# Kernel tuning notes

Measured on AMD Instinct MI355X. Metric: run time of the kernel, lower is better.

The kernel has to match this reference:

```python
import math
import jax, jax.numpy as jnp
import numpy as np

B, T, D, H = 4, 2048, 1024, 16
HD = D // H


def setup_inputs() -> dict:
    key = jax.random.key(0)
    ks = jax.random.split(key, 5)
    s = 1.0 / math.sqrt(D)  # linear-layer-ish init scale
    x = jax.random.normal(ks[0], (B, T, D), dtype=jnp.float32)
    wq = jax.random.normal(ks[1], (D, D), dtype=jnp.float32) * s
    wk = jax.random.normal(ks[2], (D, D), dtype=jnp.float32) * s
    wv = jax.random.normal(ks[3], (D, D), dtype=jnp.float32) * s
    wo = jax.random.normal(ks[4], (D, D), dtype=jnp.float32) * s
    bq = jnp.zeros((D,), jnp.float32)
    bk = jnp.zeros((D,), jnp.float32)
    bv = jnp.zeros((D,), jnp.float32)
    bo = jnp.zeros((D,), jnp.float32)
    # causal 0/1 mask, broadcast over batch and heads: [1, 1, T, T]
    mask = jnp.tril(jnp.ones((T, T), jnp.int32))[None, None]
    return {"x": x, "wq": wq, "bq": bq, "wk": wk, "bk": bk,
            "wv": wv, "bv": bv, "wo": wo, "bo": bo, "mask": mask}


def reference(x, wq, bq, wk, bk, wv, bv, wo, bo, mask):
    b, t, d = x.shape
    # separate QKV linears (x_cond defaults to x -> self-attention)
    q = x @ wq.T + bq
    k = x @ wk.T + bk
    v = x @ wv.T + bv
    # [b, t, h, hd] -> [b, h, t, hd]
    q = q.reshape(b, t, H, HD).transpose(0, 2, 1, 3)
    k = k.reshape(b, t, H, HD).transpose(0, 2, 1, 3)
    v = v.reshape(b, t, H, HD).transpose(0, 2, 1, 3)
    scale = 1.0 / math.sqrt(HD)
    attn = jnp.einsum('bhtd,bhsd->bhts', q, k) * scale  # [b, h, t, t]
    attn = jnp.where(mask[:, :, :t, :t] == 0, jnp.float32(-jnp.inf), attn)
    attn = jax.nn.softmax(attn, axis=-1)
    # dropout is identity in eval mode
    out = jnp.einsum('bhts,bhsd->bhtd', attn, v)  # [b, h, t, hd]
    out = out.transpose(0, 2, 1, 3).reshape(b, t, d)
    return out @ wo.T + bo
```

## Files before the change

kernel.cpp:

```cpp
#include <hip/hip_runtime.h>
#include <cstdint>

typedef __bf16 bf16x8 __attribute__((ext_vector_type(8)));
typedef float f32x4 __attribute__((ext_vector_type(4)));
typedef uint32_t u32x4 __attribute__((ext_vector_type(4)));
typedef unsigned short u16;

#define B_ 4
#define T_ 2048
#define D_ 1024
#define H_ 16
#define HD_ 64
#define M_ (B_*T_)
#define QSCALE 0.1803368801111204f

__device__ __forceinline__ u16 f2bf(float f) {
  union { float f; uint32_t u; } x; x.f = f;
  uint32_t u = x.u;
  uint32_t r = (u + 0x7FFFu + ((u >> 16) & 1u)) >> 16;
  return (u16)r;
}

__device__ __forceinline__ uint32_t pkbf(float a, float b) {
  union { float f; uint32_t u; } x, y; x.f = a; y.f = b;
  uint32_t t0 = x.u + 0x8000u, t1 = y.u + 0x8000u;
  return __builtin_amdgcn_perm(t1, t0, 0x07060302u);
}

__device__ __forceinline__ bf16x8 ld8(const u16* p) {
  return *(const bf16x8*)p;
}

__device__ __forceinline__ void gl_lds16(const u16* g, u16* l) {
  __builtin_amdgcn_global_load_lds(
      (__attribute__((address_space(1))) void*)(g),
      (__attribute__((address_space(3))) void*)(l), 16, 0, 0);
}

__global__ void cvt_all(const float* __restrict__ x, const float* __restrict__ wq,
                        const float* __restrict__ wk, const float* __restrict__ wv,
                        const float* __restrict__ wo,
                        u16* __restrict__ xb, u16* __restrict__ wqb, u16* __restrict__ wkb,
                        u16* __restrict__ wvb, u16* __restrict__ wob) {
  const long NX = (long)M_ * D_;
  long i = ((long)blockIdx.x * 256 + threadIdx.x) * 4;
  const float* s; u16* d; long j;
  if (i < NX) { s = x; d = xb; j = i; }
  else {
    long r = i - NX; int seg = (int)(r >> 20); j = r & ((1 << 20) - 1);
    s = seg == 0 ? wq : seg == 1 ? wk : seg == 2 ? wv : wo;
    d = seg == 0 ? wqb : seg == 1 ? wkb : seg == 2 ? wvb : wob;
  }
  float4 v = *(const float4*)(s + j);
  ushort4 o;
  o.x = f2bf(v.x); o.y = f2bf(v.y); o.z = f2bf(v.z); o.w = f2bf(v.w);
  *(ushort4*)(d + j) = o;
}


__device__ __forceinline__ void ldA_all(bf16x8 (&af)[4][2], const u16* buf,
                                        int wr, int lanem, int quad) {
#pragma unroll
  for (int mi = 0; mi < 4; ++mi)
#pragma unroll
    for (int ks = 0; ks < 2; ++ks) {
      int row = wr * 64 + mi * 16 + lanem;
      int off = row * 64 + ((ks * 32 + quad * 8) ^ ((lanem & 7) << 3));
      af[mi][ks] = ld8(buf + off);
    }
}

__device__ __forceinline__ void ldB_all(bf16x8 (&bfr)[4][2], const u16* buf,
                                        int wc, int lanem, int quad) {
#pragma unroll
  for (int nj = 0; nj < 4; ++nj)
#pragma unroll
    for (int ks = 0; ks < 2; ++ks) {
      int row = 256 + wc * 64 + nj * 16 + lanem;
      int off = row * 64 + ((ks * 32 + quad * 8) ^ ((lanem & 7) << 3));
      bfr[nj][ks] = ld8(buf + off);
    }
}

__device__ __forceinline__ void mfmaAll(f32x4 (&acc)[4][4], const bf16x8 (&af)[4][2],
                                        const bf16x8 (&bfr)[4][2]) {
#pragma unroll
  for (int mi = 0; mi < 4; ++mi)
#pragma unroll
    for (int nj = 0; nj < 4; ++nj)
#pragma unroll
      for (int ks = 0; ks < 2; ++ks)
        acc[mi][nj] = __builtin_amdgcn_mfma_f32_16x16x32_bf16(
            af[mi][ks], bfr[nj][ks], acc[mi][nj], 0, 0, 0);
}

#define GEMM_V5_KLOOP(Asrc, Bsrc)                                              \
  u16* p0 = &sm.S[0][0][0];                                                    \
  u16* p1 = &sm.S[1][0][0];                                                    \
  u16* p2 = &sm.S[2][0][0];                                                    \
  auto stage = [&](u16* bufbase, int u, int k0) {                              \
    const u16* src = (u < 4)                                                   \
        ? Asrc + (size_t)(m0 + u * 64 + wv * 8 + grow) * D_ + k0 + gcol        \
        : Bsrc + (size_t)(n0 + (u - 4) * 64 + wv * 8 + grow) * D_ + k0 + gcol; \
    gl_lds16(src, bufbase + (u * 64 + wv * 8) * 64);                           \
  };                                                                           \
  _Pragma("unroll")                                                            \
  for (int u = 0; u < 6; ++u) stage(p0, u, 0);                                 \
  _Pragma("unroll")                                                            \
  for (int u = 0; u < 6; ++u) stage(p1, u, 64);                                \
  asm volatile("s_waitcnt vmcnt(6)" ::: "memory");                             \
  __builtin_amdgcn_s_barrier();                                                \
  for (int kt = 0; kt < 16; ++kt) {                                            \
    const int k2 = (kt + 2) << 6;                                              \
    ldA_all(af, p0, wr, lanem, quad);                                          \
    ldB_all(bfr, p0, wc, lanem, quad);                                         \
    if (kt < 14) {                                                             \
      stage(p2, 0, k2); stage(p2, 1, k2); stage(p2, 2, k2);                    \
      stage(p2, 3, k2); stage(p2, 4, k2); stage(p2, 5, k2);                    \
    }                                                                          \
    asm volatile("s_waitcnt lgkmcnt(0)" ::: "memory");                         \
    __builtin_amdgcn_sched_barrier(0);                                         \
    __builtin_amdgcn_s_setprio(1);                                             \
    mfmaAll(acc, af, bfr);                                                     \
    __builtin_amdgcn_s_setprio(0);                                             \
    __builtin_amdgcn_sched_barrier(0);                                         \
    if (kt < 14)       asm volatile("s_waitcnt vmcnt(6)" ::: "memory");        \
    else if (kt == 14) asm volatile("s_waitcnt vmcnt(0)" ::: "memory");        \
    __builtin_amdgcn_s_barrier();                                              \
    u16* t = p0; p0 = p1; p1 = p2; p2 = t;                                     \
  }

__global__ __launch_bounds__(512, 2)
void gemm_qkv(const u16* __restrict__ A, const u16* __restrict__ Bw,
              const float* __restrict__ bq, const float* __restrict__ bk,
              const float* __restrict__ bv,
              u16* __restrict__ qb, u16* __restrict__ kb, u16* __restrict__ vtb) {
  __shared__ union {
    u16 S[3][384][64];
    u16 C[256 * 136];
  } sm;

  const int tid = threadIdx.x;
  const int wv = tid >> 6, lane = tid & 63;
  const int lanem = lane & 15, quad = lane >> 4;
  const int wr = wv >> 1, wc = wv & 1;

  const int l = ((int)blockIdx.x & 7) * 96 + ((int)blockIdx.x >> 3);
  const int n0 = (l % 24) * 128, m0 = (l / 24) * 256;

  const int grow = lane >> 3;
  const int gcol = (((lane & 7) ^ grow) * 8);

  f32x4 acc[4][4];
#pragma unroll
  for (int a = 0; a < 4; ++a)
#pragma unroll
    for (int b = 0; b < 4; ++b) acc[a][b] = (f32x4){0.f, 0.f, 0.f, 0.f};

  bf16x8 af[4][2];
  bf16x8 bfr[4][2];

  GEMM_V5_KLOOP(A, Bw);

  const int seg = n0 >> 10, n0l = n0 & 1023;
  const int bb = m0 >> 11, tl0 = m0 & (T_ - 1);

  if (seg == 2) {
    __syncthreads();
#pragma unroll
    for (int a = 0; a < 4; ++a)
#pragma unroll
      for (int nj = 0; nj < 4; ++nj) {
        int ncol = wc * 64 + nj * 16 + lanem;
        float bvv = bv[n0l + ncol];
        int mb = wr * 64 + a * 16 + quad * 4;
        ushort4 w4;
        w4.x = f2bf(acc[a][nj][0] + bvv);
        w4.y = f2bf(acc[a][nj][1] + bvv);
        w4.z = f2bf(acc[a][nj][2] + bvv);
        w4.w = f2bf(acc[a][nj][3] + bvv);
        *(ushort4*)&sm.C[ncol * 264 + mb] = w4;
      }
    __syncthreads();
#pragma unroll
    for (int it = 0; it < 8; ++it) {
      int chunk = it * 512 + tid;
      int nrow = chunk >> 5, c8 = chunk & 31;
      int gnl = n0l + nrow;
      int hh = gnl >> 6, hd = gnl & 63;
      *(uint4*)&vtb[(((size_t)bb * H_ + hh) * HD_ + hd) * T_ + tl0 + c8 * 8] =
          *(const uint4*)&sm.C[nrow * 264 + c8 * 8];
    }
  } else {
    const float* bias = seg == 0 ? bq : bk;
    u16* out = seg == 0 ? qb : kb;
    const float sc = seg == 0 ? QSCALE : 1.0f;
    __syncthreads();
#pragma unroll
    for (int a = 0; a < 4; ++a)
#pragma unroll
      for (int nj = 0; nj < 4; ++nj) {
        int col = wc * 64 + nj * 16 + lanem;
        float bvv = bias[n0l + col];
        int r = wr * 64 + a * 16 + quad * 4;
#pragma unroll
        for (int i = 0; i < 4; ++i)
          sm.C[(r + i) * 136 + col] = f2bf((acc[a][nj][i] + bvv) * sc);
      }
    __syncthreads();
#pragma unroll
    for (int it = 0; it < 8; ++it) {
      int chunk = it * 512 + tid;
      int row = chunk >> 4, c8 = chunk & 15;
      int col0 = c8 * 8;
      int hh = (n0l + col0) >> 6, hd = col0 & 63;
      int t = tl0 + row;
      *(uint4*)&out[(((size_t)bb * H_ + hh) * T_ + t) * HD_ + hd] =
          *(const uint4*)&sm.C[row * 136 + col0];
    }
  }
}

__global__ __launch_bounds__(512, 2)
void gemm_wo(const u16* __restrict__ A, const u16* __restrict__ Bw,
             const float* __restrict__ bias, float* __restrict__ Co) {
  __shared__ union {
    u16 S[3][384][64];
    u16 C[256 * 136];
  } sm;

  const int tid = threadIdx.x;
  const int wv = tid >> 6, lane = tid & 63;
  const int lanem = lane & 15, quad = lane >> 4;
  const int wr = wv >> 1, wc = wv & 1;

  const int l = ((int)blockIdx.x & 7) * 32 + ((int)blockIdx.x >> 3);
  const int n0 = (l & 7) * 128, m0 = (l >> 3) * 256;

  const int grow = lane >> 3;
  const int gcol = (((lane & 7) ^ grow) * 8);

  f32x4 acc[4][4];
#pragma unroll
  for (int a = 0; a < 4; ++a)
#pragma unroll
    for (int b = 0; b < 4; ++b) acc[a][b] = (f32x4){0.f, 0.f, 0.f, 0.f};

  bf16x8 af[4][2];
  bf16x8 bfr[4][2];

  GEMM_V5_KLOOP(A, Bw);

#pragma unroll
  for (int nj = 0; nj < 4; ++nj) {
    int gn = n0 + wc * 64 + nj * 16 + lanem;
    float bvv = bias[gn];
#pragma unroll
    for (int a = 0; a < 4; ++a)
#pragma unroll
      for (int i = 0; i < 4; ++i) {
        int gm = m0 + wr * 64 + a * 16 + quad * 4 + i;
        Co[(size_t)gm * D_ + gn] = acc[a][nj][i] + bvv;
      }
  }
}

__global__ __launch_bounds__(256, 4)
void flash4(const u16* __restrict__ qb, const u16* __restrict__ kb,
            const u16* __restrict__ vtb, u16* __restrict__ ob) {
  __shared__ u16 Ks[2][2][64][32];
  __shared__ u16 Vs[2][2][64][32];
  int tid = threadIdx.x, wv = tid >> 6, lane = tid & 63;
  int lanem = lane & 15, quad = lane >> 4;
  int h = blockIdx.y, b = blockIdx.z;
  int z = (int)blockIdx.z;
  int qt = ((int)blockIdx.x ^ ((z & 1) * 15) ^ ((z >> 1) * 3)) & 15;
  size_t bh = (size_t)b * H_ + h;
  int qrow0 = qt * 128 + wv * 32;
  const u16* Qg = qb + (bh * T_ + qrow0) * HD_;
  const u16* Kg = kb + bh * T_ * HD_;
  const u16* Vg = vtb + bh * HD_ * T_;

  int slot = tid >> 2, r = slot & 15;
  int key = (slot >> 5) * 32 + (r >> 2) * 8 + ((slot >> 4) & 1) * 4 + (r & 3);
  const u16* gK = Kg + (size_t)key * HD_ + (tid & 3) * 8;
  const u16* gV = Vg + (size_t)slot * T_ + (tid & 3) * 8;

  bf16x8 bq[2][2];
#pragma unroll
  for (int mi = 0; mi < 2; ++mi)
#pragma unroll
    for (int ks = 0; ks < 2; ++ks)
      bq[mi][ks] = ld8(&Qg[(size_t)(mi * 16 + lanem) * HD_ + ks * 32 + quad * 8]);

  f32x4 acc_o[2][4];
  float lsum[2][4];
#pragma unroll
  for (int mi = 0; mi < 2; ++mi) {
#pragma unroll
    for (int c = 0; c < 4; ++c) lsum[mi][c] = 0.f;
#pragma unroll
    for (int ni = 0; ni < 4; ++ni) acc_o[mi][ni] = (f32x4){0.f, 0.f, 0.f, 0.f};
  }

  int nIter = qt * 2 + 2;
  int myTiles = (qrow0 >> 6) + 1;

#define STAGE_KV(bufi, s0c)                                                 \
  do {                                                                      \
    gl_lds16(gK + (size_t)(s0c) * HD_,      &Ks[bufi][0][0][0] + wv * 512); \
    gl_lds16(gK + (size_t)(s0c) * HD_ + 32, &Ks[bufi][1][0][0] + wv * 512); \
    gl_lds16(gV + (s0c),                    &Vs[bufi][0][0][0] + wv * 512); \
    gl_lds16(gV + (s0c) + 32,               &Vs[bufi][1][0][0] + wv * 512); \
  } while (0)

  STAGE_KV(0, 0);
  for (int it = 0; it < nIter; ++it) {
    __builtin_amdgcn_s_waitcnt(0);
    __syncthreads();
    if (it + 1 < nIter) STAGE_KV((it + 1) & 1, (it + 1) * 64);
    if (it >= myTiles) continue;
    int s0 = it * 64, buf = it & 1;

    f32x4 accs[2][4];
#pragma unroll
    for (int mi = 0; mi < 2; ++mi)
#pragma unroll
      for (int ni = 0; ni < 4; ++ni) accs[mi][ni] = (f32x4){0.f, 0.f, 0.f, 0.f};
    __builtin_amdgcn_s_setprio(1);
#pragma unroll
    for (int ks = 0; ks < 2; ++ks)
#pragma unroll
      for (int ni = 0; ni < 4; ++ni) {
        bf16x8 kf = ld8(&Ks[buf][ks][ni * 16 + lanem][quad * 8]);
        accs[0][ni] = __builtin_amdgcn_mfma_f32_16x16x32_bf16(kf, bq[0][ks], accs[0][ni], 0, 0, 0);
        accs[1][ni] = __builtin_amdgcn_mfma_f32_16x16x32_bf16(kf, bq[1][ks], accs[1][ni], 0, 0, 0);
      }
    __builtin_amdgcn_s_setprio(0);

    if (s0 + 63 > qrow0) {
#pragma unroll
      for (int mi = 0; mi < 2; ++mi) {
        int qg = qrow0 + mi * 16 + lanem;
#pragma unroll
        for (int ni = 0; ni < 4; ++ni)
#pragma unroll
          for (int i = 0; i < 4; ++i) {
            int sl = (ni >> 1) * 32 + quad * 8 + (ni & 1) * 4 + i;
            float p = (s0 + sl > qg) ? 0.f : __builtin_amdgcn_exp2f(accs[mi][ni][i]);
            accs[mi][ni][i] = p;
            lsum[mi][i] += p;
          }
      }
    } else {
#pragma unroll
      for (int mi = 0; mi < 2; ++mi)
#pragma unroll
        for (int ni = 0; ni < 4; ++ni)
#pragma unroll
          for (int i = 0; i < 4; ++i) {
            float p = __builtin_amdgcn_exp2f(accs[mi][ni][i]);
            accs[mi][ni][i] = p;
            lsum[mi][i] += p;
          }
    }

#pragma unroll
    for (int c = 0; c < 2; ++c) {
      u32x4 pk0, pk1;
      pk0[0] = pkbf(accs[0][c * 2][0], accs[0][c * 2][1]);
      pk0[1] = pkbf(accs[0][c * 2][2], accs[0][c * 2][3]);
      pk0[2] = pkbf(accs[0][c * 2 + 1][0], accs[0][c * 2 + 1][1]);
      pk0[3] = pkbf(accs[0][c * 2 + 1][2], accs[0][c * 2 + 1][3]);
      pk1[0] = pkbf(accs[1][c * 2][0], accs[1][c * 2][1]);
      pk1[1] = pkbf(accs[1][c * 2][2], accs[1][c * 2][3]);
      pk1[2] = pkbf(accs[1][c * 2 + 1][0], accs[1][c * 2 + 1][1]);
      pk1[3] = pkbf(accs[1][c * 2 + 1][2], accs[1][c * 2 + 1][3]);
      bf16x8 bp0 = __builtin_bit_cast(bf16x8, pk0);
      bf16x8 bp1 = __builtin_bit_cast(bf16x8, pk1);
      __builtin_amdgcn_s_setprio(1);
#pragma unroll
      for (int ni = 0; ni < 4; ++ni) {
        bf16x8 vf = ld8(&Vs[buf][c][ni * 16 + lanem][quad * 8]);
        acc_o[0][ni] = __builtin_amdgcn_mfma_f32_16x16x32_bf16(vf, bp0, acc_o[0][ni], 0, 0, 0);
        acc_o[1][ni] = __builtin_amdgcn_mfma_f32_16x16x32_bf16(vf, bp1, acc_o[1][ni], 0, 0, 0);
      }
      __builtin_amdgcn_s_setprio(0);
    }
  }
#undef STAGE_KV

#pragma unroll
  for (int mi = 0; mi < 2; ++mi) {
    float v = (lsum[mi][0] + lsum[mi][1]) + (lsum[mi][2] + lsum[mi][3]);
    v += __shfl_xor(v, 16);
    v += __shfl_xor(v, 32);
    float inv = 1.f / v;
    int q = qrow0 + mi * 16 + lanem;
    u16* og = ob + ((size_t)b * T_ + q) * D_ + h * HD_;
#pragma unroll
    for (int ni = 0; ni < 4; ++ni) {
      ushort4 st;
      st.x = f2bf(acc_o[mi][ni][0] * inv);
      st.y = f2bf(acc_o[mi][ni][1] * inv);
      st.z = f2bf(acc_o[mi][ni][2] * inv);
      st.w = f2bf(acc_o[mi][ni][3] * inv);
      *(ushort4*)(og + ni * 16 + quad * 4) = st;
    }
  }
}

extern "C" void kernel_launch(void* const* d_in, const int* in_sizes, int n_in,
                              void* d_out, int out_size, void* d_ws, size_t ws_size,
                              hipStream_t stream) {
  const float* x  = (const float*)d_in[0];
  const float* wq = (const float*)d_in[1];
  const float* bq = (const float*)d_in[2];
  const float* wk = (const float*)d_in[3];
  const float* bk = (const float*)d_in[4];
  const float* wv = (const float*)d_in[5];
  const float* bv = (const float*)d_in[6];
  const float* wo = (const float*)d_in[7];
  const float* bo = (const float*)d_in[8];

  char* ws = (char*)d_ws;
  const size_t MB = 1ull << 20;
  u16* xb   = (u16*)(ws + 0 * MB);
  u16* wqkv = (u16*)(ws + 16 * MB);
  u16* wob  = (u16*)(ws + 22 * MB);
  u16* qb   = (u16*)(ws + 24 * MB);
  u16* kb   = (u16*)(ws + 40 * MB);
  u16* vtb  = (u16*)(ws + 56 * MB);
  u16* ob   = (u16*)(ws + 72 * MB);

  cvt_all<<<(M_ * D_ + 4 * D_ * D_) / 1024, 256, 0, stream>>>(
      x, wq, wk, wv, wo, xb, wqkv, wqkv + (size_t)D_ * D_, wqkv + 2 * (size_t)D_ * D_, wob);

  gemm_qkv<<<768, 512, 0, stream>>>(xb, wqkv, bq, bk, bv, qb, kb, vtb);

  flash4<<<dim3(T_ / 128, H_, B_), 256, 0, stream>>>(qb, kb, vtb, ob);

  gemm_wo<<<256, 512, 0, stream>>>(ob, wob, bo, (float*)d_out);
}
```

Before: 257.8 us.

## Rewrite QKV GEMM k-loop as 4-stage BK=32 pipeline with register double-buffering

The QKV projection GEMM moves from a 3-buffer BK=64 LDS pipeline to a 4-buffer BK=32 pipeline. It prefetches the next k-step's fragments into double-buffered registers while the current MFMAs run, and uses a new XOR swizzle for the 32-wide rows. This aims to hide LDS read latency behind MFMA work and keep more global loads in flight. The attention kernel also drops its s_setprio raises around the MFMA blocks. Twice as many k-iterations add more barriers, and the extra fragment registers increase register pressure.

```diff
diff --git a/kernel.cpp b/kernel.cpp
--- a/kernel.cpp
+++ b/kernel.cpp
@@ -55,6 +55,147 @@
   ushort4 o;
   o.x = f2bf(v.x); o.y = f2bf(v.y); o.z = f2bf(v.z); o.w = f2bf(v.w);
   *(ushort4*)(d + j) = o;
+}
+
+
+__global__ __launch_bounds__(512, 2)
+void gemm_qkv(const u16* __restrict__ A, const u16* __restrict__ Bw,
+              const float* __restrict__ bq, const float* __restrict__ bk,
+              const float* __restrict__ bv,
+              u16* __restrict__ qb, u16* __restrict__ kb, u16* __restrict__ vtb) {
+  __shared__ union {
+    u16 S[4][384][32];
+    u16 C[256 * 136];
+  } sm;
+
+  const int tid = threadIdx.x;
+  const int wv = tid >> 6, lane = tid & 63;
+  const int lanem = lane & 15, quad = lane >> 4;
+  const int wr = wv >> 1, wc = wv & 1;
+
+  const int l = ((int)blockIdx.x & 7) * 96 + ((int)blockIdx.x >> 3);
+  const int n0 = (l % 24) * 128, m0 = (l / 24) * 256;
+
+  const int srow = lane >> 2;
+  const int schunk = (lane & 3) ^ ((srow >> 1) & 3);
+
+  auto stage = [&](int bufi, int kt) {
+    const int k0 = kt << 5;
+    u16* base = &sm.S[bufi][0][0];
+#pragma unroll
+    for (int u = 0; u < 3; ++u) {
+      const u16* src = (u < 2)
+          ? A  + (size_t)(m0 + u * 128 + wv * 16 + srow) * D_ + k0 + schunk * 8
+          : Bw + (size_t)(n0 + wv * 16 + srow) * D_ + k0 + schunk * 8;
+      gl_lds16(src, base + (u * 128 + wv * 16) * 32);
+    }
+  };
+
+  const int rsw = (quad ^ ((lanem >> 1) & 3)) * 8;
+  auto ldfrag = [&](bf16x8 (&af)[4], bf16x8 (&bf)[4], int bufi) {
+    const u16* base = &sm.S[bufi][0][0];
+#pragma unroll
+    for (int mi = 0; mi < 4; ++mi)
+      af[mi] = ld8(base + (wr * 64 + mi * 16 + lanem) * 32 + rsw);
+#pragma unroll
+    for (int nj = 0; nj < 4; ++nj)
+      bf[nj] = ld8(base + (256 + wc * 64 + nj * 16 + lanem) * 32 + rsw);
+  };
+
+  f32x4 acc[4][4];
+#pragma unroll
+  for (int a = 0; a < 4; ++a)
+#pragma unroll
+    for (int b = 0; b < 4; ++b) acc[a][b] = (f32x4){0.f, 0.f, 0.f, 0.f};
+
+  bf16x8 afr[2][4], bfr[2][4];
+
+  stage(0, 0); stage(1, 1); stage(2, 2);
+  asm volatile("s_waitcnt vmcnt(3)" ::: "memory");
+  __builtin_amdgcn_s_barrier();
+  __builtin_amdgcn_sched_barrier(0);
+  ldfrag(afr[0], bfr[0], 0);
+
+#pragma unroll 2
+  for (int kt = 0; kt < 32; ++kt) {
+    const int cur = kt & 1;
+    if (kt < 31) ldfrag(afr[cur ^ 1], bfr[cur ^ 1], (kt + 1) & 3);
+    if (kt < 29) stage((kt + 3) & 3, kt + 3);
+    if (kt < 31) asm volatile("s_waitcnt lgkmcnt(8)" ::: "memory");
+    else         asm volatile("s_waitcnt lgkmcnt(0)" ::: "memory");
+    __builtin_amdgcn_sched_barrier(0);
+    __builtin_amdgcn_s_setprio(1);
+#pragma unroll
+    for (int mi = 0; mi < 4; ++mi)
+#pragma unroll
+      for (int nj = 0; nj < 4; ++nj)
+        acc[mi][nj] = __builtin_amdgcn_mfma_f32_16x16x32_bf16(
+            afr[cur][mi], bfr[cur][nj], acc[mi][nj], 0, 0, 0);
+    __builtin_amdgcn_s_setprio(0);
+    __builtin_amdgcn_sched_barrier(0);
+    if (kt < 29)       asm volatile("s_waitcnt vmcnt(3)" ::: "memory");
+    else if (kt == 29) asm volatile("s_waitcnt vmcnt(0)" ::: "memory");
+    __builtin_amdgcn_s_barrier();
+    __builtin_amdgcn_sched_barrier(0);
+  }
+
+  const int seg = n0 >> 10, n0l = n0 & 1023;
+  const int bb = m0 >> 11, tl0 = m0 & (T_ - 1);
+
+  if (seg == 2) {
+    __syncthreads();
+#pragma unroll
+    for (int a = 0; a < 4; ++a)
+#pragma unroll
+      for (int nj = 0; nj < 4; ++nj) {
+        int ncol = wc * 64 + nj * 16 + lanem;
+        float bvv = bv[n0l + ncol];
+        int mb = wr * 64 + a * 16 + quad * 4;
+        ushort4 w4;
+        w4.x = f2bf(acc[a][nj][0] + bvv);
+        w4.y = f2bf(acc[a][nj][1] + bvv);
+        w4.z = f2bf(acc[a][nj][2] + bvv);
+        w4.w = f2bf(acc[a][nj][3] + bvv);
+        *(ushort4*)&sm.C[ncol * 264 + mb] = w4;
+      }
+    __syncthreads();
+#pragma unroll
+    for (int it = 0; it < 8; ++it) {
+      int chunk = it * 512 + tid;
+      int nrow = chunk >> 5, c8 = chunk & 31;
+      int gnl = n0l + nrow;
+      int hh = gnl >> 6, hd = gnl & 63;
+      *(uint4*)&vtb[(((size_t)bb * H_ + hh) * HD_ + hd) * T_ + tl0 + c8 * 8] =
+          *(const uint4*)&sm.C[nrow * 264 + c8 * 8];
+    }
+  } else {
+    const float* bias = seg == 0 ? bq : bk;
+    u16* out = seg == 0 ? qb : kb;
+    const float sc = seg == 0 ? QSCALE : 1.0f;
+    __syncthreads();
+#pragma unroll
+    for (int a = 0; a < 4; ++a)
+#pragma unroll
+      for (int nj = 0; nj < 4; ++nj) {
+        int col = wc * 64 + nj * 16 + lanem;
+        float bvv = bias[n0l + col];
+        int r = wr * 64 + a * 16 + quad * 4;
+#pragma unroll
+        for (int i = 0; i < 4; ++i)
+          sm.C[(r + i) * 136 + col] = f2bf((acc[a][nj][i] + bvv) * sc);
+      }
+    __syncthreads();
+#pragma unroll
+    for (int it = 0; it < 8; ++it) {
+      int chunk = it * 512 + tid;
+      int row = chunk >> 4, c8 = chunk & 15;
+      int col0 = c8 * 8;
+      int hh = (n0l + col0) >> 6, hd = col0 & 63;
+      int t = tl0 + row;
+      *(uint4*)&out[(((size_t)bb * H_ + hh) * T_ + t) * HD_ + hd] =
+          *(const uint4*)&sm.C[row * 136 + col0];
+    }
+  }
 }
 
 
@@ -131,97 +272,6 @@
   }
 
 __global__ __launch_bounds__(512, 2)
-void gemm_qkv(const u16* __restrict__ A, const u16* __restrict__ Bw,
-              const float* __restrict__ bq, const float* __restrict__ bk,
-              const float* __restrict__ bv,
-              u16* __restrict__ qb, u16* __restrict__ kb, u16* __restrict__ vtb) {
-  __shared__ union {
-    u16 S[3][384][64];
-    u16 C[256 * 136];
-  } sm;
-
-  const int tid = threadIdx.x;
-  const int wv = tid >> 6, lane = tid & 63;
-  const int lanem = lane & 15, quad = lane >> 4;
-  const int wr = wv >> 1, wc = wv & 1;
-
-  const int l = ((int)blockIdx.x & 7) * 96 + ((int)blockIdx.x >> 3);
-  const int n0 = (l % 24) * 128, m0 = (l / 24) * 256;
-
-  const int grow = lane >> 3;
-  const int gcol = (((lane & 7) ^ grow) * 8);
-
-  f32x4 acc[4][4];
-#pragma unroll
-  for (int a = 0; a < 4; ++a)
-#pragma unroll
-    for (int b = 0; b < 4; ++b) acc[a][b] = (f32x4){0.f, 0.f, 0.f, 0.f};
-
-  bf16x8 af[4][2];
-  bf16x8 bfr[4][2];
-
-  GEMM_V5_KLOOP(A, Bw);
-
-  const int seg = n0 >> 10, n0l = n0 & 1023;
-  const int bb = m0 >> 11, tl0 = m0 & (T_ - 1);
-
-  if (seg == 2) {
-    __syncthreads();
-#pragma unroll
-    for (int a = 0; a < 4; ++a)
-#pragma unroll
-      for (int nj = 0; nj < 4; ++nj) {
-        int ncol = wc * 64 + nj * 16 + lanem;
-        float bvv = bv[n0l + ncol];
-        int mb = wr * 64 + a * 16 + quad * 4;
-        ushort4 w4;
-        w4.x = f2bf(acc[a][nj][0] + bvv);
-        w4.y = f2bf(acc[a][nj][1] + bvv);
-        w4.z = f2bf(acc[a][nj][2] + bvv);
-        w4.w = f2bf(acc[a][nj][3] + bvv);
-        *(ushort4*)&sm.C[ncol * 264 + mb] = w4;
-      }
-    __syncthreads();
-#pragma unroll
-    for (int it = 0; it < 8; ++it) {
-      int chunk = it * 512 + tid;
-      int nrow = chunk >> 5, c8 = chunk & 31;
-      int gnl = n0l + nrow;
-      int hh = gnl >> 6, hd = gnl & 63;
-      *(uint4*)&vtb[(((size_t)bb * H_ + hh) * HD_ + hd) * T_ + tl0 + c8 * 8] =
-          *(const uint4*)&sm.C[nrow * 264 + c8 * 8];
-    }
-  } else {
-    const float* bias = seg == 0 ? bq : bk;
-    u16* out = seg == 0 ? qb : kb;
-    const float sc = seg == 0 ? QSCALE : 1.0f;
-    __syncthreads();
-#pragma unroll
-    for (int a = 0; a < 4; ++a)
-#pragma unroll
-      for (int nj = 0; nj < 4; ++nj) {
-        int col = wc * 64 + nj * 16 + lanem;
-        float bvv = bias[n0l + col];
-        int r = wr * 64 + a * 16 + quad * 4;
-#pragma unroll
-        for (int i = 0; i < 4; ++i)
-          sm.C[(r + i) * 136 + col] = f2bf((acc[a][nj][i] + bvv) * sc);
-      }
-    __syncthreads();
-#pragma unroll
-    for (int it = 0; it < 8; ++it) {
-      int chunk = it * 512 + tid;
-      int row = chunk >> 4, c8 = chunk & 15;
-      int col0 = c8 * 8;
-      int hh = (n0l + col0) >> 6, hd = col0 & 63;
-      int t = tl0 + row;
-      *(uint4*)&out[(((size_t)bb * H_ + hh) * T_ + t) * HD_ + hd] =
-          *(const uint4*)&sm.C[row * 136 + col0];
-    }
-  }
-}
-
-__global__ __launch_bounds__(512, 2)
 void gemm_wo(const u16* __restrict__ A, const u16* __restrict__ Bw,
              const float* __restrict__ bias, float* __restrict__ Co) {
   __shared__ union {
@@ -327,7 +377,6 @@
     for (int mi = 0; mi < 2; ++mi)
 #pragma unroll
       for (int ni = 0; ni < 4; ++ni) accs[mi][ni] = (f32x4){0.f, 0.f, 0.f, 0.f};
-    __builtin_amdgcn_s_setprio(1);
 #pragma unroll
     for (int ks = 0; ks < 2; ++ks)
 #pragma unroll
@@ -336,7 +385,6 @@
         accs[0][ni] = __builtin_amdgcn_mfma_f32_16x16x32_bf16(kf, bq[0][ks], accs[0][ni], 0, 0, 0);
         accs[1][ni] = __builtin_amdgcn_mfma_f32_16x16x32_bf16(kf, bq[1][ks], accs[1][ni], 0, 0, 0);
       }
-    __builtin_amdgcn_s_setprio(0);
 
     if (s0 + 63 > qrow0) {
 #pragma unroll
@@ -378,14 +426,12 @@
       pk1[3] = pkbf(accs[1][c * 2 + 1][2], accs[1][c * 2 + 1][3]);
       bf16x8 bp0 = __builtin_bit_cast(bf16x8, pk0);
       bf16x8 bp1 = __builtin_bit_cast(bf16x8, pk1);
-      __builtin_amdgcn_s_setprio(1);
 #pragma unroll
       for (int ni = 0; ni < 4; ++ni) {
         bf16x8 vf = ld8(&Vs[buf][c][ni * 16 + lanem][quad * 8]);
         acc_o[0][ni] = __builtin_amdgcn_mfma_f32_16x16x32_bf16(vf, bp0, acc_o[0][ni], 0, 0, 0);
         acc_o[1][ni] = __builtin_amdgcn_mfma_f32_16x16x32_bf16(vf, bp1, acc_o[1][ni], 0, 0, 0);
       }
-      __builtin_amdgcn_s_setprio(0);
     }
   }
 #undef STAGE_KV
```

After: 261.7 us. Within noise of the previous version (+1.5%).
